# Performance work log

Measured on AMD Instinct MI355X. Metric: run time of the kernel, lower is better.

Reference implementation:

```python
import jax, jax.numpy as jnp
import numpy as np

N = 50000      # nodes
E = 1600000    # edges (avg degree 32)
D = 64         # d_node
DE = 32        # d_edge
H = 4          # heads
L = 3          # layers


def _ln(x, g, b):
    mu = x.mean(-1, keepdims=True)
    var = ((x - mu) ** 2).mean(-1, keepdims=True)
    return (x - mu) / jnp.sqrt(var + 1e-5) * g + b


def setup_inputs() -> dict:
    key = jax.random.key(0)
    ks = jax.random.split(key, 16)
    s = 0.05
    return {
        "node_features": jax.random.normal(ks[0], (N, D), jnp.float32),
        "edge_features": jax.random.normal(ks[1], (E, DE), jnp.float32),
        "edge_index": jax.random.randint(ks[2], (2, E), 0, N),
        "Wq": jax.random.normal(ks[3], (L, D, D), jnp.float32) * s,
        "Wk": jax.random.normal(ks[4], (L, D, D), jnp.float32) * s,
        "Wv": jax.random.normal(ks[5], (L, D, D), jnp.float32) * s,
        "Wo": jax.random.normal(ks[6], (L, D, D), jnp.float32) * s,
        "We": jax.random.normal(ks[7], (L, DE, H), jnp.float32) * s,   # edge-conditioned score bias
        "Wem": jax.random.normal(ks[8], (L, 2 * D + DE, DE), jnp.float32) * s,
        "bem": jnp.zeros((L, DE), jnp.float32),
        "gn": jnp.ones((L, D), jnp.float32),
        "bn": jnp.zeros((L, D), jnp.float32),
        "ge": jnp.ones((L, DE), jnp.float32),
        "be": jnp.zeros((L, DE), jnp.float32),
    }


def _delta_forward(h, e, src, dst, Wq, Wk, Wv, Wo, We, Wem, bem, gn, bn, ge, be):
    n = h.shape[0]
    dh = D // H
    for i in range(L):
        # --- node attention over edges (sparse, per-dst segment softmax) ---
        q = (h @ Wq[i]).reshape(n, H, dh)
        k = (h @ Wk[i]).reshape(n, H, dh)
        v = (h @ Wv[i]).reshape(n, H, dh)
        scores = jnp.einsum('ehd,ehd->eh', q[dst], k[src]) / jnp.sqrt(jnp.float32(dh))
        scores = scores + e @ We[i]                         # edge-conditioned bias [E,H]
        m = jax.ops.segment_max(scores, dst, num_segments=n)
        p = jnp.exp(scores - m[dst])
        denom = jax.ops.segment_sum(p, dst, num_segments=n)
        alpha = p / (denom[dst] + 1e-9)                      # [E,H]
        msg = (alpha[:, :, None] * v[src]).reshape(-1, D)    # [E,D]
        agg = jax.ops.segment_sum(msg, dst, num_segments=n)  # [N,D]
        h = _ln(h + agg @ Wo[i], gn[i], bn[i])
        # --- edge update conditioned on endpoint nodes ---
        emsg = jax.nn.gelu(jnp.concatenate([h[src], h[dst], e], axis=-1) @ Wem[i] + bem[i])
        e = _ln(e + emsg, ge[i], be[i])
    return h


def reference(node_features, edge_features, edge_index, Wq, Wk, Wv, Wo, We, Wem, bem, gn, bn, ge, be):
    src = edge_index[0]
    dst = edge_index[1]
    return _delta_forward(node_features, edge_features, src, dst,
                          Wq, Wk, Wv, Wo, We, Wem, bem, gn, bn, ge, be)
```

## Files before the change

### kernel.cpp

```cpp
#include <hip/hip_runtime.h>
#include <hip/hip_bf16.h>
#include <math.h>

#define NN 50000
#define NE 1600000
#define D 64
#define DE 32
#define H 4
#define DH 16
#define L 3

typedef __attribute__((ext_vector_type(8))) short bf16x8;
typedef __attribute__((ext_vector_type(8))) short s16x8;
typedef __attribute__((ext_vector_type(4))) float f32x4;

__device__ __forceinline__ short f2b(float f) {
    __hip_bfloat16 h = __float2bfloat16(f);
    short s;
    __builtin_memcpy(&s, &h, 2);
    return s;
}
__device__ __forceinline__ float b2f(unsigned short u) {
    unsigned int x = ((unsigned int)u) << 16;
    float f; __builtin_memcpy(&f, &x, 4); return f;
}
__device__ __forceinline__ float b2f_lo(unsigned int p) {
    unsigned int x = p << 16;
    float f; __builtin_memcpy(&f, &x, 4); return f;
}
__device__ __forceinline__ float b2f_hi(unsigned int p) {
    unsigned int x = p & 0xffff0000u;
    float f; __builtin_memcpy(&f, &x, 4); return f;
}


__global__ void deg_kernel(const int* __restrict__ dst, int* __restrict__ cnt) {
    int e = blockIdx.x * 256 + threadIdx.x;
    if (e >= NE) return;
    atomicAdd(&cnt[dst[e]], 1);
}

__global__ void block_sum_kernel(const int* __restrict__ cnt, int* __restrict__ bsum) {
    int b = blockIdx.x, t = threadIdx.x;
    int base = b * 1024 + t * 4;
    int s = 0;
#pragma unroll
    for (int i = 0; i < 4; i++) { int idx = base + i; if (idx < NN) s += cnt[idx]; }
#pragma unroll
    for (int off = 32; off; off >>= 1) s += __shfl_down(s, off);
    __shared__ int wsum[4];
    if ((t & 63) == 0) wsum[t >> 6] = s;
    __syncthreads();
    if (t == 0) bsum[b] = wsum[0] + wsum[1] + wsum[2] + wsum[3];
}

__global__ void scan_bsum_kernel(int* __restrict__ bsum, int nb) {
    if (blockIdx.x == 0 && threadIdx.x == 0) {
        int run = 0;
        for (int i = 0; i < nb; i++) { int c = bsum[i]; bsum[i] = run; run += c; }
    }
}

__global__ void scan_block_kernel(const int* __restrict__ cnt, const int* __restrict__ bsum,
                                  int* __restrict__ offsets) {
    int b = blockIdx.x, t = threadIdx.x;
    int base = b * 1024 + t * 4;
    int v[4]; int s = 0;
#pragma unroll
    for (int i = 0; i < 4; i++) { int idx = base + i; v[i] = (idx < NN) ? cnt[idx] : 0; s += v[i]; }
    int lane = t & 63, w = t >> 6;
    int x = s;
#pragma unroll
    for (int off = 1; off < 64; off <<= 1) {
        int y = __shfl_up(x, off);
        if (lane >= off) x += y;
    }
    __shared__ int wsum[4];
    if (lane == 63) wsum[w] = x;
    __syncthreads();
    int woff = 0;
    for (int i = 0; i < w; i++) woff += wsum[i];
    int run = bsum[b] + woff + x - s;
#pragma unroll
    for (int i = 0; i < 4; i++) {
        int idx = base + i;
        if (idx < NN) offsets[idx] = run;
        run += v[i];
    }
}

__global__ void scatter_kernel(const int* __restrict__ src, const int* __restrict__ dst,
                               const int* __restrict__ offsets,
                               int* __restrict__ cursor,
                               int* __restrict__ sorted_eid,
                               int* __restrict__ sorted_src,
                               int* __restrict__ sorted_dst) {
    int e = blockIdx.x * 256 + threadIdx.x;
    if (e >= NE) return;
    int d0 = dst[e];
    int pos = atomicAdd(&cursor[d0], 1);
    int position = offsets[d0] + pos;
    sorted_eid[position] = e;
    sorted_src[position] = src[e];
    sorted_dst[position] = d0;
}

__global__ void eperm_kernel(const float* __restrict__ e32, const int* __restrict__ sorted_eid,
                             const float* __restrict__ We0,
                             unsigned short* __restrict__ eb_s,
                             float* __restrict__ ebias_s) {
    int t = blockIdx.x * 256 + threadIdx.x;
    if (t >= NE * 4) return;
    int p = t >> 2;
    int c = (t & 3) * 8;
    int eid = sorted_eid[p];
    const float* ep = e32 + (size_t)eid * DE + c;
    float4 x0 = *(const float4*)(ep);
    float4 x1 = *(const float4*)(ep + 4);
    float e8[8] = {x0.x, x0.y, x0.z, x0.w, x1.x, x1.y, x1.z, x1.w};
    s16x8 ob;
#pragma unroll
    for (int i = 0; i < 8; i++) ob[i] = f2b(e8[i]);
    *(s16x8*)(eb_s + (size_t)p * DE + c) = ob;
    float p0 = 0.f, p1 = 0.f, p2 = 0.f, p3 = 0.f;
#pragma unroll
    for (int i = 0; i < 8; i++) {
        float4 w = *(const float4*)(We0 + (c + i) * 4);
        p0 += e8[i] * w.x; p1 += e8[i] * w.y; p2 += e8[i] * w.z; p3 += e8[i] * w.w;
    }
#pragma unroll
    for (int off = 1; off < 4; off <<= 1) {
        p0 += __shfl_xor(p0, off, 4);
        p1 += __shfl_xor(p1, off, 4);
        p2 += __shfl_xor(p2, off, 4);
        p3 += __shfl_xor(p3, off, 4);
    }
    if ((t & 3) == 0) {
        float4 o; o.x = p0; o.y = p1; o.z = p2; o.w = p3;
        *(float4*)(ebias_s + (size_t)p * H) = o;
    }
}

__global__ void wconv_kernel(const float* __restrict__ Wem, unsigned short* __restrict__ Wt) {
    int t = blockIdx.x * 256 + threadIdx.x;
    if (t >= L * 32 * 160) return;
    int l = t / 5120;
    int r = t % 5120;
    int n = r / 160;
    int k = r % 160;
    Wt[t] = (unsigned short)f2b(Wem[l * 5120 + k * 32 + n]);
}

__global__ void hconv_kernel(const float* __restrict__ nf, float* __restrict__ h,
                             unsigned short* __restrict__ hb) {
    int t = blockIdx.x * 256 + threadIdx.x;
    if (t >= NN * D) return;
    float x = nf[t];
    h[t] = x;
    hb[t] = (unsigned short)f2b(x);
}


__global__ void qkv_kernel(const float* __restrict__ h,
                           const float* __restrict__ Wq,
                           const float* __restrict__ Wk,
                           const float* __restrict__ Wv,
                           float* __restrict__ q, unsigned int* __restrict__ kv) {
    __shared__ float sW[3 * 4096];
    __shared__ float sh[16][D];
    int col = threadIdx.x;
    int wv = threadIdx.y;
    int tid = wv * 64 + col;
    int base = blockIdx.x * 16;
    for (int i = tid; i < 4096; i += 256) {
        sW[i] = Wq[i]; sW[4096 + i] = Wk[i]; sW[8192 + i] = Wv[i];
    }
    for (int i = tid; i < 16 * D; i += 256) {
        int n = base + (i >> 6);
        sh[i >> 6][i & 63] = h[n * D + (i & 63)];
    }
    __syncthreads();
#pragma unroll
    for (int it = 0; it < 4; it++) {
        int ln = wv * 4 + it;
        int node = base + ln;
        float aq = 0.f, ak = 0.f, av = 0.f;
#pragma unroll
        for (int kk = 0; kk < D; kk++) {
            float hv = sh[ln][kk];
            aq += hv * sW[kk * D + col];
            ak += hv * sW[4096 + kk * D + col];
            av += hv * sW[8192 + kk * D + col];
        }
        q[node * D + col] = aq * 0.25f;
        unsigned int kb = (unsigned int)(unsigned short)f2b(ak);
        unsigned int vb = (unsigned int)(unsigned short)f2b(av);
        kv[node * D + col] = (vb << 16) | kb;
    }
}

__global__ void attn_kernel(const float* __restrict__ q, const unsigned int* __restrict__ kv,
                            const float* __restrict__ ebias_s,
                            const int* __restrict__ sorted_src,
                            const int* __restrict__ offsets,
                            float* __restrict__ agg) {
    int node = blockIdx.x * 4 + threadIdx.y;
    node = __builtin_amdgcn_readfirstlane(node);
    if (node >= NN) return;
    int lane = threadIdx.x;
    int hh = lane >> 4;
    float qv = q[node * D + lane];
    int beg = offsets[node];
    int end = (node == NN - 1) ? NE : offsets[node + 1];
    float mmax = -INFINITY, den = 0.f, acc = 0.f;
    int i = beg;
    for (; i + 8 <= end; i += 8) {
        int ss[8]; unsigned int kk8[8]; float bb8[8], dd[8];
#pragma unroll
        for (int u = 0; u < 8; u++) ss[u] = sorted_src[i + u];
#pragma unroll
        for (int u = 0; u < 8; u++) kk8[u] = kv[ss[u] * D + lane];
#pragma unroll
        for (int u = 0; u < 8; u++) bb8[u] = ebias_s[(i + u) * H + hh];
#pragma unroll
        for (int u = 0; u < 8; u++) dd[u] = qv * b2f_lo(kk8[u]);
#pragma unroll
        for (int off = 1; off < 16; off <<= 1) {
#pragma unroll
            for (int u = 0; u < 8; u++) dd[u] += __shfl_xor(dd[u], off, 16);
        }
        float nm = mmax;
#pragma unroll
        for (int u = 0; u < 8; u++) { dd[u] += bb8[u]; nm = fmaxf(nm, dd[u]); }
        float scale = __expf(mmax - nm);
        float ps = 0.f, av = 0.f;
#pragma unroll
        for (int u = 0; u < 8; u++) {
            float p = __expf(dd[u] - nm);
            ps += p;
            av += p * b2f_hi(kk8[u]);
        }
        den = den * scale + ps;
        acc = acc * scale + av;
        mmax = nm;
    }
    for (; i < end; i++) {
        int s = sorted_src[i];
        unsigned int kvv = kv[s * D + lane];
        float b = ebias_s[i * H + hh];
        float dot = qv * b2f_lo(kvv);
#pragma unroll
        for (int off = 1; off < 16; off <<= 1) dot += __shfl_xor(dot, off, 16);
        float score = dot + b;
        float nm = fmaxf(mmax, score);
        float scale = __expf(mmax - nm);
        float p = __expf(score - nm);
        den = den * scale + p;
        acc = acc * scale + p * b2f_hi(kvv);
        mmax = nm;
    }
    agg[node * D + lane] = acc / (den + 1e-9f);
}

__global__ void node_update_kernel(float* __restrict__ h, const float* __restrict__ agg,
                                   const float* __restrict__ Wo,
                                   const float* __restrict__ gn,
                                   const float* __restrict__ bn,
                                   unsigned short* __restrict__ hb) {
    __shared__ float sWo[4096];
    __shared__ float sagg[16][D];
    int col = threadIdx.x, wv = threadIdx.y;
    int tid = wv * 64 + col;
    int base = blockIdx.x * 16;
    for (int i = tid; i < 4096; i += 256) sWo[i] = Wo[i];
    for (int i = tid; i < 16 * D; i += 256) {
        int n = base + (i >> 6);
        sagg[i >> 6][i & 63] = agg[n * D + (i & 63)];
    }
    __syncthreads();
    float gcol = gn[col], bcol = bn[col];
#pragma unroll
    for (int it = 0; it < 4; it++) {
        int ln = wv * 4 + it;
        int node = base + ln;
        float acc = 0.f;
#pragma unroll
        for (int kk = 0; kk < D; kk++) acc += sagg[ln][kk] * sWo[kk * D + col];
        float x = h[node * D + col] + acc;
        float sum = x, sq = x * x;
#pragma unroll
        for (int off = 32; off; off >>= 1) {
            sum += __shfl_xor(sum, off);
            sq += __shfl_xor(sq, off);
        }
        float mu = sum * (1.f / 64.f);
        float var = sq * (1.f / 64.f) - mu * mu;
        float out = (x - mu) * rsqrtf(var + 1e-5f) * gcol + bcol;
        h[node * D + col] = out;
        hb[node * D + col] = (unsigned short)f2b(out);
    }
}

__global__ __launch_bounds__(256, 4)
void edge_update_mfma_kernel(const unsigned short* __restrict__ hb,
                             unsigned short* __restrict__ eb_s,
                             const int* __restrict__ sorted_src,
                             const int* __restrict__ sorted_dst,
                             const unsigned short* __restrict__ Wt,
                             const float* __restrict__ bem,
                             const float* __restrict__ ge,
                             const float* __restrict__ be,
                             const float* __restrict__ We_next,
                             float* __restrict__ ebias_s,
                             int do_bias, int do_estore) {
    __shared__ __align__(16) unsigned short sWt[32][168];
    __shared__ __align__(16) float ytr[4][16][36];
    int tid = threadIdx.x;
    int wave = tid >> 6;
    int lane = tid & 63;
    int we = blockIdx.x * 64 + wave * 16;
    int m = lane & 15;
    int quad = lane >> 4;
    int p_m = we + m;
    int s_idx = sorted_src[p_m], d_idx = sorted_dst[p_m];

    const unsigned short* as = hb + (size_t)s_idx * D + quad * 8;
    const unsigned short* ad = hb + (size_t)d_idx * D + quad * 8;
    bf16x8 a_s0 = *(const bf16x8*)(as);
    bf16x8 a_s1 = *(const bf16x8*)(as + 32);
    bf16x8 a_d0 = *(const bf16x8*)(ad);
    bf16x8 a_d1 = *(const bf16x8*)(ad + 32);
    bf16x8 ea = *(const bf16x8*)(eb_s + (size_t)p_m * DE + quad * 8);

    {
        const unsigned int* Wt32 = (const unsigned int*)Wt;
#pragma unroll
        for (int it = 0; it < 10; it++) {
            int i = tid + it * 256;
            int sh = i * 2;
            int r = sh / 160, c = sh % 160;
            *(unsigned int*)&sWt[r][c] = Wt32[i];
        }
    }

    bf16x8 wb;
#pragma unroll
    for (int j = 0; j < 8; j++) {
        float w = (do_bias && m < 4) ? We_next[(quad * 8 + j) * 4 + m] : 0.f;
        wb[j] = f2b(w);
    }

    __syncthreads();

    f32x4 c0 = {0.f, 0.f, 0.f, 0.f};
    f32x4 c1 = {0.f, 0.f, 0.f, 0.f};
    const unsigned short* w0 = &sWt[m][quad * 8];
    const unsigned short* w1 = &sWt[m + 16][quad * 8];

#pragma unroll
    for (int ks = 0; ks < 4; ks++) {
        bf16x8 a = (ks == 0) ? a_s0 : (ks == 1) ? a_s1 : (ks == 2) ? a_d0 : a_d1;
        bf16x8 b0 = *(const bf16x8*)(w0 + ks * 32);
        bf16x8 b1 = *(const bf16x8*)(w1 + ks * 32);
        c0 = __builtin_amdgcn_mfma_f32_16x16x32_bf16(a, b0, c0, 0, 0, 0);
        c1 = __builtin_amdgcn_mfma_f32_16x16x32_bf16(a, b1, c1, 0, 0, 0);
    }
    {
        bf16x8 b0 = *(const bf16x8*)(w0 + 4 * 32);
        bf16x8 b1 = *(const bf16x8*)(w1 + 4 * 32);
        c0 = __builtin_amdgcn_mfma_f32_16x16x32_bf16(ea, b0, c0, 0, 0, 0);
        c1 = __builtin_amdgcn_mfma_f32_16x16x32_bf16(ea, b1, c1, 0, 0, 0);
    }

    float bm0 = bem[m], bm1 = bem[m + 16];
#pragma unroll
    for (int reg = 0; reg < 4; reg++) {
        int row = quad * 4 + reg;
        float y0 = c0[reg] + bm0;
        float y1 = c1[reg] + bm1;
        float u0 = 1.5957691216057308f * (y0 + 0.044715f * y0 * y0 * y0);
        float u1 = 1.5957691216057308f * (y1 + 0.044715f * y1 * y1 * y1);
        float t0 = 1.f - 2.f / (1.f + __expf(u0));
        float t1 = 1.f - 2.f / (1.f + __expf(u1));
        ytr[wave][row][m] = 0.5f * y0 * (1.f + t0);
        ytr[wave][row][m + 16] = 0.5f * y1 * (1.f + t1);
    }
    __syncthreads();

    float y[8];
    *(f32x4*)&y[0] = *(const f32x4*)&ytr[wave][m][quad * 8];
    *(f32x4*)&y[4] = *(const f32x4*)&ytr[wave][m][quad * 8 + 4];
    float s = 0.f, sq = 0.f;
#pragma unroll
    for (int j = 0; j < 8; j++) {
        y[j] += b2f((unsigned short)ea[j]);
        s += y[j];
        sq += y[j] * y[j];
    }
    s += __shfl_xor(s, 16); s += __shfl_xor(s, 32);
    sq += __shfl_xor(sq, 16); sq += __shfl_xor(sq, 32);
    float mu = s * (1.f / 32.f);
    float var = sq * (1.f / 32.f) - mu * mu;
    float inv = rsqrtf(var + 1e-5f);

    float4 g0 = *(const float4*)(ge + quad * 8);
    float4 g1 = *(const float4*)(ge + quad * 8 + 4);
    float4 b0 = *(const float4*)(be + quad * 8);
    float4 b1 = *(const float4*)(be + quad * 8 + 4);
    float gg[8] = {g0.x, g0.y, g0.z, g0.w, g1.x, g1.y, g1.z, g1.w};
    float bbv[8] = {b0.x, b0.y, b0.z, b0.w, b1.x, b1.y, b1.z, b1.w};
    bf16x8 zb;
#pragma unroll
    for (int j = 0; j < 8; j++) {
        float z = (y[j] - mu) * inv * gg[j] + bbv[j];
        zb[j] = f2b(z);
    }
    if (do_estore) {
        *(s16x8*)(eb_s + (size_t)p_m * DE + quad * 8) = zb;
    }
    if (do_bias) {
        f32x4 db = {0.f, 0.f, 0.f, 0.f};
        db = __builtin_amdgcn_mfma_f32_16x16x32_bf16(zb, wb, db, 0, 0, 0);
        if (m < 4) {
#pragma unroll
            for (int reg = 0; reg < 4; reg++) {
                ebias_s[(we + quad * 4 + reg) * H + m] = db[reg];
            }
        }
    }
}

extern "C" void kernel_launch(void* const* d_in, const int* in_sizes, int n_in,
                              void* d_out, int out_size, void* d_ws, size_t ws_size,
                              hipStream_t stream) {
    const float* node_features = (const float*)d_in[0];
    const float* e = (const float*)d_in[1];
    const int* edge_index = (const int*)d_in[2];
    const int* src = edge_index;
    const int* dst = edge_index + NE;
    const float* Wq = (const float*)d_in[3];
    const float* Wk = (const float*)d_in[4];
    const float* Wv = (const float*)d_in[5];
    const float* Wo = (const float*)d_in[6];
    const float* We = (const float*)d_in[7];
    const float* Wem = (const float*)d_in[8];
    const float* bem = (const float*)d_in[9];
    const float* gn = (const float*)d_in[10];
    const float* bn = (const float*)d_in[11];
    const float* ge = (const float*)d_in[12];
    const float* be = (const float*)d_in[13];

    float* h = (float*)d_out;

    float* ws = (float*)d_ws;
    float* q = ws;
    unsigned int* kv = (unsigned int*)(q + NN * D);
    float* agg = (float*)(kv + NN * D);
    float* ebias_s = agg + NN * D;
    int* offsets = (int*)(ebias_s + (size_t)NE * H);
    int* cursor = offsets + NN;
    int* bsum = cursor + NN;
    int* sorted_eid = bsum + 64;
    int* sorted_src = sorted_eid + NE;
    int* sorted_dst = sorted_src + NE;
    unsigned short* Wt = (unsigned short*)(sorted_dst + NE);
    unsigned short* hb = Wt + L * 32 * 160;
    unsigned short* eb_s = hb + NN * D;

    const int NB = (NN + 1023) / 1024;

    hipMemsetAsync(cursor, 0, NN * sizeof(int), stream);
    deg_kernel<<<(NE + 255) / 256, 256, 0, stream>>>(dst, cursor);
    block_sum_kernel<<<NB, 256, 0, stream>>>(cursor, bsum);
    scan_bsum_kernel<<<1, 64, 0, stream>>>(bsum, NB);
    scan_block_kernel<<<NB, 256, 0, stream>>>(cursor, bsum, offsets);
    hipMemsetAsync(cursor, 0, NN * sizeof(int), stream);
    scatter_kernel<<<(NE + 255) / 256, 256, 0, stream>>>(src, dst, offsets, cursor,
                                                         sorted_eid, sorted_src, sorted_dst);
    eperm_kernel<<<(NE * 4 + 255) / 256, 256, 0, stream>>>(e, sorted_eid, We, eb_s, ebias_s);
    wconv_kernel<<<(L * 32 * 160 + 255) / 256, 256, 0, stream>>>(Wem, Wt);
    hconv_kernel<<<(NN * D + 255) / 256, 256, 0, stream>>>(node_features, h, hb);

    for (int layer = 0; layer < L; layer++) {
        const float* Wq_l = Wq + layer * D * D;
        const float* Wk_l = Wk + layer * D * D;
        const float* Wv_l = Wv + layer * D * D;
        const float* Wo_l = Wo + layer * D * D;
        const unsigned short* Wt_l = Wt + layer * 32 * 160;
        const float* bem_l = bem + layer * DE;
        const float* gn_l = gn + layer * D;
        const float* bn_l = bn + layer * D;
        const float* ge_l = ge + layer * DE;
        const float* be_l = be + layer * DE;

        qkv_kernel<<<NN / 16, dim3(64, 4), 0, stream>>>(h, Wq_l, Wk_l, Wv_l, q, kv);
        attn_kernel<<<NN / 4, dim3(64, 4), 0, stream>>>(q, kv, ebias_s, sorted_src,
                                                        offsets, agg);
        node_update_kernel<<<NN / 16, dim3(64, 4), 0, stream>>>(h, agg, Wo_l,
                                                                gn_l, bn_l, hb);
        if (layer < L - 1) {
            const float* We_next = We + (layer + 1) * DE * H;
            edge_update_mfma_kernel<<<NE / 64, 256, 0, stream>>>(hb, eb_s, sorted_src,
                                                                 sorted_dst, Wt_l,
                                                                 bem_l, ge_l, be_l,
                                                                 We_next, ebias_s,
                                                                 1, layer == 0 ? 1 : 0);
        }
    }
}
```

Before: 1.230 ms.

## Use split-bf16 MFMA for QKV and output projections instead of scalar FMA

Pre-splits Wq/Wk/Wv/Wo into transposed bf16 hi/lo pairs once, then computes the per-node QKV and Wo projections with 16x16x32 bf16 MFMA using a three-term hi/lo product to keep near-fp32 accuracy. This drops the 48KB/16KB shared-memory weight staging per block and the scalar FMA loops, which should raise occupancy and throughput. It drops the lo*lo term, which adds a small rounding error, and these node kernels are only a modest share of total time next to the edge kernels.

```diff
diff --git a/kernel.cpp b/kernel.cpp
--- a/kernel.cpp
+++ b/kernel.cpp
@@ -151,6 +151,24 @@
     Wt[t] = (unsigned short)f2b(Wem[l * 5120 + k * 32 + n]);
 }
 
+__global__ void wsplit_kernel(const float* __restrict__ Wq, const float* __restrict__ Wk,
+                              const float* __restrict__ Wv, const float* __restrict__ Wo,
+                              unsigned short* __restrict__ WT_hi,
+                              unsigned short* __restrict__ WT_lo) {
+    int t = blockIdx.x * 256 + threadIdx.x;
+    if (t >= L * 4 * 64 * 64) return;
+    int k = t & 63;
+    int n = (t >> 6) & 63;
+    int mat = (t >> 12) & 3;
+    int l = t >> 14;
+    const float* W = (mat == 0) ? Wq : (mat == 1) ? Wk : (mat == 2) ? Wv : Wo;
+    float w = W[l * 4096 + k * 64 + n];
+    unsigned short hi = (unsigned short)f2b(w);
+    float lo = w - b2f(hi);
+    WT_hi[t] = hi;
+    WT_lo[t] = (unsigned short)f2b(lo);
+}
+
 __global__ void hconv_kernel(const float* __restrict__ nf, float* __restrict__ h,
                              unsigned short* __restrict__ hb) {
     int t = blockIdx.x * 256 + threadIdx.x;
@@ -161,41 +179,58 @@
 }
 
 
-__global__ void qkv_kernel(const float* __restrict__ h,
-                           const float* __restrict__ Wq,
-                           const float* __restrict__ Wk,
-                           const float* __restrict__ Wv,
-                           float* __restrict__ q, unsigned int* __restrict__ kv) {
-    __shared__ float sW[3 * 4096];
-    __shared__ float sh[16][D];
-    int col = threadIdx.x;
-    int wv = threadIdx.y;
-    int tid = wv * 64 + col;
+__global__ __launch_bounds__(256, 8)
+void qkv_kernel(const float* __restrict__ h,
+                const unsigned short* __restrict__ WT_hi,
+                const unsigned short* __restrict__ WT_lo,
+                float* __restrict__ q, unsigned int* __restrict__ kv) {
+    int lane = threadIdx.x & 63;
+    int wv = threadIdx.x >> 6;
+    int m = lane & 15, quad = lane >> 4;
     int base = blockIdx.x * 16;
-    for (int i = tid; i < 4096; i += 256) {
-        sW[i] = Wq[i]; sW[4096 + i] = Wk[i]; sW[8192 + i] = Wv[i];
-    }
-    for (int i = tid; i < 16 * D; i += 256) {
-        int n = base + (i >> 6);
-        sh[i >> 6][i & 63] = h[n * D + (i & 63)];
-    }
-    __syncthreads();
-#pragma unroll
-    for (int it = 0; it < 4; it++) {
-        int ln = wv * 4 + it;
-        int node = base + ln;
-        float aq = 0.f, ak = 0.f, av = 0.f;
-#pragma unroll
-        for (int kk = 0; kk < D; kk++) {
-            float hv = sh[ln][kk];
-            aq += hv * sW[kk * D + col];
-            ak += hv * sW[4096 + kk * D + col];
-            av += hv * sW[8192 + kk * D + col];
-        }
-        q[node * D + col] = aq * 0.25f;
-        unsigned int kb = (unsigned int)(unsigned short)f2b(ak);
-        unsigned int vb = (unsigned int)(unsigned short)f2b(av);
-        kv[node * D + col] = (vb << 16) | kb;
+
+    const float* hp = h + (size_t)(base + m) * D + quad * 8;
+    float af[16];
+    *(f32x4*)&af[0]  = *(const f32x4*)(hp);
+    *(f32x4*)&af[4]  = *(const f32x4*)(hp + 4);
+    *(f32x4*)&af[8]  = *(const f32x4*)(hp + 32);
+    *(f32x4*)&af[12] = *(const f32x4*)(hp + 36);
+    bf16x8 a0h, a0l, a1h, a1l;
+#pragma unroll
+    for (int j = 0; j < 8; j++) {
+        short h0 = f2b(af[j]);
+        short h1 = f2b(af[8 + j]);
+        a0h[j] = h0; a0l[j] = f2b(af[j] - b2f((unsigned short)h0));
+        a1h[j] = h1; a1l[j] = f2b(af[8 + j] - b2f((unsigned short)h1));
+    }
+
+    f32x4 acc[3];
+#pragma unroll
+    for (int mat = 0; mat < 3; mat++) {
+        const unsigned short* bh = WT_hi + ((size_t)mat * 64 + wv * 16 + m) * 64 + quad * 8;
+        const unsigned short* bl = WT_lo + ((size_t)mat * 64 + wv * 16 + m) * 64 + quad * 8;
+        bf16x8 bh0 = *(const bf16x8*)(bh);
+        bf16x8 bh1 = *(const bf16x8*)(bh + 32);
+        bf16x8 bl0 = *(const bf16x8*)(bl);
+        bf16x8 bl1 = *(const bf16x8*)(bl + 32);
+        f32x4 c = {0.f, 0.f, 0.f, 0.f};
+        c = __builtin_amdgcn_mfma_f32_16x16x32_bf16(a0h, bh0, c, 0, 0, 0);
+        c = __builtin_amdgcn_mfma_f32_16x16x32_bf16(a1h, bh1, c, 0, 0, 0);
+        c = __builtin_amdgcn_mfma_f32_16x16x32_bf16(a0h, bl0, c, 0, 0, 0);
+        c = __builtin_amdgcn_mfma_f32_16x16x32_bf16(a1h, bl1, c, 0, 0, 0);
+        c = __builtin_amdgcn_mfma_f32_16x16x32_bf16(a0l, bh0, c, 0, 0, 0);
+        c = __builtin_amdgcn_mfma_f32_16x16x32_bf16(a1l, bh1, c, 0, 0, 0);
+        acc[mat] = c;
+    }
+
+#pragma unroll
+    for (int reg = 0; reg < 4; reg++) {
+        int row = base + quad * 4 + reg;
+        int col = wv * 16 + m;
+        q[(size_t)row * D + col] = acc[0][reg] * 0.25f;
+        unsigned int kb = (unsigned short)f2b(acc[1][reg]);
+        unsigned int vb = (unsigned short)f2b(acc[2][reg]);
+        kv[(size_t)row * D + col] = (vb << 16) | kb;
     }
 }
 
@@ -262,31 +297,61 @@
     agg[node * D + lane] = acc / (den + 1e-9f);
 }
 
-__global__ void node_update_kernel(float* __restrict__ h, const float* __restrict__ agg,
-                                   const float* __restrict__ Wo,
-                                   const float* __restrict__ gn,
-                                   const float* __restrict__ bn,
-                                   unsigned short* __restrict__ hb) {
-    __shared__ float sWo[4096];
-    __shared__ float sagg[16][D];
-    int col = threadIdx.x, wv = threadIdx.y;
-    int tid = wv * 64 + col;
+__global__ __launch_bounds__(256, 8)
+void node_update_kernel(float* __restrict__ h, const float* __restrict__ agg,
+                        const unsigned short* __restrict__ WoT_hi,
+                        const unsigned short* __restrict__ WoT_lo,
+                        const float* __restrict__ gn,
+                        const float* __restrict__ bn,
+                        unsigned short* __restrict__ hb) {
+    __shared__ float sx[16][68];
+    int lane = threadIdx.x & 63;
+    int wv = threadIdx.x >> 6;
+    int m = lane & 15, quad = lane >> 4;
     int base = blockIdx.x * 16;
-    for (int i = tid; i < 4096; i += 256) sWo[i] = Wo[i];
-    for (int i = tid; i < 16 * D; i += 256) {
-        int n = base + (i >> 6);
-        sagg[i >> 6][i & 63] = agg[n * D + (i & 63)];
+
+    const float* ap = agg + (size_t)(base + m) * D + quad * 8;
+    float af[16];
+    *(f32x4*)&af[0]  = *(const f32x4*)(ap);
+    *(f32x4*)&af[4]  = *(const f32x4*)(ap + 4);
+    *(f32x4*)&af[8]  = *(const f32x4*)(ap + 32);
+    *(f32x4*)&af[12] = *(const f32x4*)(ap + 36);
+    bf16x8 a0h, a0l, a1h, a1l;
+#pragma unroll
+    for (int j = 0; j < 8; j++) {
+        short h0 = f2b(af[j]);
+        short h1 = f2b(af[8 + j]);
+        a0h[j] = h0; a0l[j] = f2b(af[j] - b2f((unsigned short)h0));
+        a1h[j] = h1; a1l[j] = f2b(af[8 + j] - b2f((unsigned short)h1));
+    }
+    const unsigned short* bh = WoT_hi + ((size_t)wv * 16 + m) * 64 + quad * 8;
+    const unsigned short* bl = WoT_lo + ((size_t)wv * 16 + m) * 64 + quad * 8;
+    bf16x8 bh0 = *(const bf16x8*)(bh);
+    bf16x8 bh1 = *(const bf16x8*)(bh + 32);
+    bf16x8 bl0 = *(const bf16x8*)(bl);
+    bf16x8 bl1 = *(const bf16x8*)(bl + 32);
+    f32x4 c = {0.f, 0.f, 0.f, 0.f};
+    c = __builtin_amdgcn_mfma_f32_16x16x32_bf16(a0h, bh0, c, 0, 0, 0);
+    c = __builtin_amdgcn_mfma_f32_16x16x32_bf16(a1h, bh1, c, 0, 0, 0);
+    c = __builtin_amdgcn_mfma_f32_16x16x32_bf16(a0h, bl0, c, 0, 0, 0);
+    c = __builtin_amdgcn_mfma_f32_16x16x32_bf16(a1h, bl1, c, 0, 0, 0);
+    c = __builtin_amdgcn_mfma_f32_16x16x32_bf16(a0l, bh0, c, 0, 0, 0);
+    c = __builtin_amdgcn_mfma_f32_16x16x32_bf16(a1l, bh1, c, 0, 0, 0);
+
+#pragma unroll
+    for (int reg = 0; reg < 4; reg++) {
+        int row = quad * 4 + reg;
+        int col = wv * 16 + m;
+        sx[row][col] = c[reg] + h[(size_t)(base + row) * D + col];
     }
     __syncthreads();
-    float gcol = gn[col], bcol = bn[col];
+
+    float gcol = gn[lane], bcol = bn[lane];
 #pragma unroll
     for (int it = 0; it < 4; it++) {
         int ln = wv * 4 + it;
         int node = base + ln;
-        float acc = 0.f;
-#pragma unroll
-        for (int kk = 0; kk < D; kk++) acc += sagg[ln][kk] * sWo[kk * D + col];
-        float x = h[node * D + col] + acc;
+        float x = sx[ln][lane];
         float sum = x, sq = x * x;
 #pragma unroll
         for (int off = 32; off; off >>= 1) {
@@ -296,8 +361,8 @@
         float mu = sum * (1.f / 64.f);
         float var = sq * (1.f / 64.f) - mu * mu;
         float out = (x - mu) * rsqrtf(var + 1e-5f) * gcol + bcol;
-        h[node * D + col] = out;
-        hb[node * D + col] = (unsigned short)f2b(out);
+        h[(size_t)node * D + lane] = out;
+        hb[(size_t)node * D + lane] = (unsigned short)f2b(out);
     }
 }
 
@@ -466,6 +531,8 @@
     unsigned short* Wt = (unsigned short*)(sorted_dst + NE);
     unsigned short* hb = Wt + L * 32 * 160;
     unsigned short* eb_s = hb + NN * D;
+    unsigned short* WT_hi = eb_s + (size_t)NE * DE;
+    unsigned short* WT_lo = WT_hi + L * 4 * 64 * 64;
 
     const int NB = (NN + 1023) / 1024;
 
@@ -479,13 +546,13 @@
                                                          sorted_eid, sorted_src, sorted_dst);
     eperm_kernel<<<(NE * 4 + 255) / 256, 256, 0, stream>>>(e, sorted_eid, We, eb_s, ebias_s);
     wconv_kernel<<<(L * 32 * 160 + 255) / 256, 256, 0, stream>>>(Wem, Wt);
+    wsplit_kernel<<<(L * 4 * 64 * 64 + 255) / 256, 256, 0, stream>>>(Wq, Wk, Wv, Wo,
+                                                                     WT_hi, WT_lo);
     hconv_kernel<<<(NN * D + 255) / 256, 256, 0, stream>>>(node_features, h, hb);
 
     for (int layer = 0; layer < L; layer++) {
-        const float* Wq_l = Wq + layer * D * D;
-        const float* Wk_l = Wk + layer * D * D;
-        const float* Wv_l = Wv + layer * D * D;
-        const float* Wo_l = Wo + layer * D * D;
+        const unsigned short* WT_hi_l = WT_hi + (size_t)layer * 4 * 4096;
+        const unsigned short* WT_lo_l = WT_lo + (size_t)layer * 4 * 4096;
         const unsigned short* Wt_l = Wt + layer * 32 * 160;
         const float* bem_l = bem + layer * DE;
         const float* gn_l = gn + layer * D;
@@ -493,11 +560,13 @@
         const float* ge_l = ge + layer * DE;
         const float* be_l = be + layer * DE;
 
-        qkv_kernel<<<NN / 16, dim3(64, 4), 0, stream>>>(h, Wq_l, Wk_l, Wv_l, q, kv);
+        qkv_kernel<<<NN / 16, 256, 0, stream>>>(h, WT_hi_l, WT_lo_l, q, kv);
         attn_kernel<<<NN / 4, dim3(64, 4), 0, stream>>>(q, kv, ebias_s, sorted_src,
                                                         offsets, agg);
-        node_update_kernel<<<NN / 16, dim3(64, 4), 0, stream>>>(h, agg, Wo_l,
-                                                                gn_l, bn_l, hb);
+        node_update_kernel<<<NN / 16, 256, 0, stream>>>(h, agg,
+                                                        WT_hi_l + 3 * 4096,
+                                                        WT_lo_l + 3 * 4096,
+                                                        gn_l, bn_l, hb);
         if (layer < L - 1) {
             const float* We_next = We + (layer + 1) * DE * H;
             edge_update_mfma_kernel<<<NE / 64, 256, 0, stream>>>(hb, eb_s, sorted_src,
```

Result: faster. 1.132 ms (-8.0%).
